# Optimization experiments

Measured on AMD Instinct MI355X. Metric: run time of the kernel, lower is better.

The kernel has to match this reference:

```python
import jax, jax.numpy as jnp
import numpy as np

ADAPTIVE_FACTOR = 10  # max(10, num_agents=8)


def _mlp(x, W1, b1, W2, b2, W3, b3):
    h = jax.nn.relu(x @ W1 + b1)
    h = jax.nn.relu(h @ W2 + b2)
    return h @ W3 + b3


def setup_inputs() -> dict:
    key = jax.random.key(0)
    ks = jax.random.split(key, 8)
    B, T, N, D, A = 32, 512, 8, 256, 64
    obs = jax.random.normal(ks[0], (B, T, N, D), dtype=jnp.float32)
    actions = jax.random.uniform(ks[1], (B, T, N, A), dtype=jnp.float32)
    din = D + A
    W1 = jax.random.normal(ks[2], (din, 128), dtype=jnp.float32) / np.sqrt(din)
    b1 = jnp.zeros((128,), dtype=jnp.float32)
    W2 = jax.random.normal(ks[3], (128, 64), dtype=jnp.float32) / np.sqrt(128.0)
    b2 = jnp.zeros((64,), dtype=jnp.float32)
    W3 = jax.random.normal(ks[4], (64, A), dtype=jnp.float32) / np.sqrt(64.0)
    b3 = jnp.zeros((A,), dtype=jnp.float32)
    return {"obs": obs, "actions": actions, "W1": W1, "b1": b1,
            "W2": W2, "b2": b2, "W3": W3, "b3": b3}


def reference(obs, actions, W1, b1, W2, b2, W3, b3):
    # obs: [B,T,N,D], actions: [B,T,N,A]. All agents processed in one batched MLP
    # pass instead of the per-agent Python loop in the original.
    p_with = _mlp(jnp.concatenate([obs, actions], axis=-1), W1, b1, W2, b2, W3, b3)
    p_wo = _mlp(jnp.concatenate([obs, jnp.zeros_like(actions)], axis=-1),
                W1, b1, W2, b2, W3, b3)

    cf_keys = jax.random.split(jax.random.key(42), ADAPTIVE_FACTOR)

    def body(acc, k):
        cf = jax.random.uniform(k, actions.shape, dtype=actions.dtype)
        return acc + _mlp(jnp.concatenate([obs, cf], axis=-1), W1, b1, W2, b2, W3, b3), None

    p_wo, _ = jax.lax.scan(body, p_wo, cf_keys)
    p_wo = p_wo / (ADAPTIVE_FACTOR + 1)

    # F.kl_div(log_softmax(p_with), softmax(p_wo), reduction='none')
    #   = q * (log q - log p)
    logp = jax.nn.log_softmax(p_with, axis=-1)
    logq = jax.nn.log_softmax(p_wo, axis=-1)
    q = jnp.exp(logq)
    influence = q * (logq - logp)          # [B,T,N,A]
    # torch: stack over agents on dim=-1 -> [B,T,A,N], then mean over dim=2 (A)
    return influence.mean(axis=-1)          # [B,T,N]
```

## Files before the change

kernel.cpp:

```cpp
#include <hip/hip_runtime.h>
#include <cstddef>

#define NCF 10

struct TFKeys { unsigned k[2 * NCF]; };

typedef __attribute__((ext_vector_type(8))) _Float16 f16x8;
typedef __attribute__((ext_vector_type(4))) float f32x4;

__host__ __device__ __forceinline__ void tf2x32(unsigned k0, unsigned k1,
                                                unsigned x0, unsigned x1,
                                                unsigned& o0, unsigned& o1) {
  const unsigned ks2 = k0 ^ k1 ^ 0x1BD11BDAu;
  x0 += k0; x1 += k1;
#define TF_R(r) x0 += x1; x1 = (x1 << (r)) | (x1 >> (32 - (r))); x1 ^= x0;
  TF_R(13) TF_R(15) TF_R(26) TF_R(6)
  x0 += k1;  x1 += ks2 + 1u;
  TF_R(17) TF_R(29) TF_R(16) TF_R(24)
  x0 += ks2; x1 += k0 + 2u;
  TF_R(13) TF_R(15) TF_R(26) TF_R(6)
  x0 += k0;  x1 += k1 + 3u;
  TF_R(17) TF_R(29) TF_R(16) TF_R(24)
  x0 += k1;  x1 += ks2 + 4u;
  TF_R(13) TF_R(15) TF_R(26) TF_R(6)
  x0 += ks2; x1 += k0 + 5u;
#undef TF_R
  o0 = x0; o1 = x1;
}

__device__ __forceinline__ float u01(unsigned bits) {
  return __uint_as_float((bits >> 9) | 0x3f800000u) - 1.0f;
}

__device__ __forceinline__ void split44(const float4 a, const float4 b,
                                        f16x8& hh, f16x8& ll) {
  const float v[8] = {a.x, a.y, a.z, a.w, b.x, b.y, b.z, b.w};
#pragma unroll
  for (int e = 0; e < 8; ++e) {
    const _Float16 h = (_Float16)v[e];
    hh[e] = h;
    ll[e] = (_Float16)(v[e] - (float)h);
  }
}

#define MFMA3(acc, ah, al, bh, bl)                                          \
  acc = __builtin_amdgcn_mfma_f32_16x16x32_f16(ah, bh, acc, 0, 0, 0);       \
  acc = __builtin_amdgcn_mfma_f32_16x16x32_f16(ah, bl, acc, 0, 0, 0);       \
  acc = __builtin_amdgcn_mfma_f32_16x16x32_f16(al, bh, acc, 0, 0, 0);

template <int K, int N>
__device__ __forceinline__ void stage_frags(const float* __restrict__ W,
                                            _Float16* fh, _Float16* fl, int t) {
  constexpr int NTN = N / 16;
  for (int i = t; i < K * N; i += 512) {
    const int e = i & 7, lane = (i >> 3) & 63, tile = i >> 9;
    const int kt = tile / NTN, nt = tile % NTN;
    const int k = kt * 32 + ((lane >> 4) << 3) + e;
    const int c = nt * 16 + (lane & 15);
    const float w = W[k * N + c];
    const _Float16 h = (_Float16)w;
    fh[i] = h;
    fl[i] = (_Float16)(w - (float)h);
  }
}

__global__ __launch_bounds__(512, 2) __attribute__((amdgpu_waves_per_eu(2, 2)))
void infl_fused(const float* __restrict__ obs, const float* __restrict__ actions,
                const float* __restrict__ W1, const float* __restrict__ b1,
                const float* __restrict__ W2, const float* __restrict__ b2,
                const float* __restrict__ W3, const float* __restrict__ b3,
                float* __restrict__ out, TFKeys keys) {
  __shared__ __align__(16) unsigned char smem[149504];
  _Float16* w1oh = (_Float16*)smem;
  _Float16* w1ol = (_Float16*)(smem + 65536);
  _Float16* w1h  = (_Float16*)smem;
  _Float16* w1l  = (_Float16*)(smem + 16384);
  _Float16* w2h  = (_Float16*)(smem + 32768);
  _Float16* w2l  = (_Float16*)(smem + 49152);
  _Float16* w3h  = (_Float16*)(smem + 65536);
  _Float16* w3l  = (_Float16*)(smem + 73728);
  float*    hbuf = (float*)(smem + 81920);

  const int t = threadIdx.x, wave = t >> 6, lane = t & 63;
  const int R0 = blockIdx.x * 128 + wave * 16;
  const int cA = lane & 15;
  const int kg = (lane >> 4) << 3;
  const int r0 = (lane >> 4) << 2;
  float* hb = hbuf + wave * 2112;

  stage_frags<256, 128>(W1, w1oh, w1ol, t);
  __syncthreads();

  f32x4 ho[8];
#pragma unroll
  for (int nt = 0; nt < 8; ++nt) {
    const float bv = b1[nt * 16 + cA];
    ho[nt] = (f32x4){bv, bv, bv, bv};
  }
  {
    const float* orow = obs + (size_t)(R0 + cA) * 256;
    float4 ov[16];
#pragma unroll
    for (int kt = 0; kt < 8; ++kt) {
      ov[2 * kt]     = *(const float4*)(orow + kt * 32 + kg);
      ov[2 * kt + 1] = *(const float4*)(orow + kt * 32 + kg + 4);
    }
#pragma unroll
    for (int kt = 0; kt < 8; ++kt) {
      f16x8 ah, al;
      split44(ov[2 * kt], ov[2 * kt + 1], ah, al);
#pragma unroll
      for (int nt = 0; nt < 8; ++nt) {
        const int tile = kt * 8 + nt;
        const f16x8 bh = *(const f16x8*)&w1oh[(tile * 64 + lane) * 8];
        const f16x8 bl = *(const f16x8*)&w1ol[(tile * 64 + lane) * 8];
        MFMA3(ho[nt], ah, al, bh, bl)
      }
    }
  }
  __syncthreads();

  stage_frags<64, 128>(W1 + 256 * 128, w1h, w1l, t);
  stage_frags<128, 64>(W2, w2h, w2l, t);
  stage_frags<64, 64>(W3, w3h, w3l, t);

  float b2r[4], b3r[4];
#pragma unroll
  for (int nt = 0; nt < 4; ++nt) {
    b2r[nt] = b2[nt * 16 + cA];
    b3r[nt] = b3[nt * 16 + cA];
  }
  __syncthreads();

#define MLP_BODY(HAS_ACT, acc3)                                              \
  {                                                                          \
    f32x4 a1[8];                                                             \
    _Pragma("unroll") for (int nt = 0; nt < 8; ++nt) a1[nt] = ho[nt];        \
    if (HAS_ACT) {                                                           \
      _Pragma("unroll") for (int kt = 0; kt < 2; ++kt)                       \
      _Pragma("unroll") for (int nt = 0; nt < 8; ++nt) {                     \
        const int tile = kt * 8 + nt;                                        \
        const f16x8 bh = *(const f16x8*)&w1h[(tile * 64 + lane) * 8];        \
        const f16x8 bl = *(const f16x8*)&w1l[(tile * 64 + lane) * 8];        \
        MFMA3(a1[nt], ah[kt], al[kt], bh, bl)                                \
      }                                                                      \
    }                                                                        \
    _Pragma("unroll") for (int nt = 0; nt < 8; ++nt)                         \
    _Pragma("unroll") for (int j = 0; j < 4; ++j)                            \
      hb[(r0 + j) * 132 + nt * 16 + cA] = fmaxf(a1[nt][j], 0.f);             \
    f32x4 a2[4];                                                             \
    _Pragma("unroll") for (int nt = 0; nt < 4; ++nt)                         \
      a2[nt] = (f32x4){b2r[nt], b2r[nt], b2r[nt], b2r[nt]};                  \
    _Pragma("unroll") for (int kt = 0; kt < 4; ++kt) {                       \
      const float4 va = *(const float4*)&hb[cA * 132 + kt * 32 + kg];        \
      const float4 vb = *(const float4*)&hb[cA * 132 + kt * 32 + kg + 4];    \
      f16x8 hh, hl;                                                          \
      split44(va, vb, hh, hl);                                               \
      _Pragma("unroll") for (int nt = 0; nt < 4; ++nt) {                     \
        const int tile = kt * 4 + nt;                                        \
        const f16x8 bh = *(const f16x8*)&w2h[(tile * 64 + lane) * 8];        \
        const f16x8 bl = *(const f16x8*)&w2l[(tile * 64 + lane) * 8];        \
        MFMA3(a2[nt], hh, hl, bh, bl)                                        \
      }                                                                      \
    }                                                                        \
    _Pragma("unroll") for (int nt = 0; nt < 4; ++nt)                         \
    _Pragma("unroll") for (int j = 0; j < 4; ++j)                            \
      hb[(r0 + j) * 68 + nt * 16 + cA] = fmaxf(a2[nt][j], 0.f);              \
    _Pragma("unroll") for (int kt = 0; kt < 2; ++kt) {                       \
      const float4 va = *(const float4*)&hb[cA * 68 + kt * 32 + kg];         \
      const float4 vb = *(const float4*)&hb[cA * 68 + kt * 32 + kg + 4];     \
      f16x8 hh, hl;                                                          \
      split44(va, vb, hh, hl);                                               \
      _Pragma("unroll") for (int nt = 0; nt < 4; ++nt) {                     \
        const int tile = kt * 4 + nt;                                        \
        const f16x8 bh = *(const f16x8*)&w3h[(tile * 64 + lane) * 8];        \
        const f16x8 bl = *(const f16x8*)&w3l[(tile * 64 + lane) * 8];        \
        MFMA3(acc3[nt], hh, hl, bh, bl)                                      \
      }                                                                      \
    }                                                                        \
  }

  f32x4 pacc[4];
#pragma unroll
  for (int nt = 0; nt < 4; ++nt) pacc[nt] = (f32x4){0.f, 0.f, 0.f, 0.f};

  for (int p = 0; p < 11; ++p) {
    f16x8 ah[2], al[2];
    if (p >= 1) {
      const unsigned k0 = keys.k[2 * (p - 1)];
      const unsigned k1 = keys.k[2 * (p - 1) + 1];
      const unsigned base = (unsigned)(R0 + cA) * 64u + (unsigned)kg;
#pragma unroll
      for (int kt = 0; kt < 2; ++kt) {
        float v[8];
#pragma unroll
        for (int e = 0; e < 8; ++e) {
          unsigned o0, o1;
          tf2x32(k0, k1, 0u, base + (unsigned)(kt * 32 + e), o0, o1);
          v[e] = u01(o0 ^ o1);
        }
        split44(*(const float4*)&v[0], *(const float4*)&v[4], ah[kt], al[kt]);
      }
    }
    MLP_BODY(p != 0, pacc)
  }

  f32x4 pw[4];
#pragma unroll
  for (int nt = 0; nt < 4; ++nt) pw[nt] = (f32x4){0.f, 0.f, 0.f, 0.f};
  {
    f16x8 ah[2], al[2];
    const float* arow = actions + (size_t)(R0 + cA) * 64 + kg;
#pragma unroll
    for (int kt = 0; kt < 2; ++kt) {
      const float4 va = *(const float4*)(arow + kt * 32);
      const float4 vb = *(const float4*)(arow + kt * 32 + 4);
      split44(va, vb, ah[kt], al[kt]);
    }
    MLP_BODY(true, pw)
  }

  const float inv11 = 1.0f / 11.0f;
#pragma unroll
  for (int j = 0; j < 4; ++j) {
    float pwv[4], pav[4];
#pragma unroll
    for (int nt = 0; nt < 4; ++nt) {
      pwv[nt] = pw[nt][j] + b3r[nt];
      pav[nt] = pacc[nt][j] * inv11 + b3r[nt];
    }
    float mw = fmaxf(fmaxf(pwv[0], pwv[1]), fmaxf(pwv[2], pwv[3]));
    float ma = fmaxf(fmaxf(pav[0], pav[1]), fmaxf(pav[2], pav[3]));
#pragma unroll
    for (int off = 1; off < 16; off <<= 1) {
      mw = fmaxf(mw, __shfl_xor(mw, off, 64));
      ma = fmaxf(ma, __shfl_xor(ma, off, 64));
    }
    float sw = 0.f, sa = 0.f;
#pragma unroll
    for (int nt = 0; nt < 4; ++nt) {
      sw += expf(pwv[nt] - mw);
      sa += expf(pav[nt] - ma);
    }
#pragma unroll
    for (int off = 1; off < 16; off <<= 1) {
      sw += __shfl_xor(sw, off, 64);
      sa += __shfl_xor(sa, off, 64);
    }
    const float lzw = logf(sw), lza = logf(sa);
    float contrib = 0.f;
#pragma unroll
    for (int nt = 0; nt < 4; ++nt) {
      const float lq = pav[nt] - ma - lza;
      const float lp = pwv[nt] - mw - lzw;
      contrib += expf(lq) * (lq - lp);
    }
#pragma unroll
    for (int off = 1; off < 16; off <<= 1)
      contrib += __shfl_xor(contrib, off, 64);
    if (cA == 0) out[R0 + r0 + j] = contrib * (1.0f / 64.0f);
  }
}

extern "C" void kernel_launch(void* const* d_in, const int* in_sizes, int n_in,
                              void* d_out, int out_size, void* d_ws, size_t ws_size,
                              hipStream_t stream) {
  (void)in_sizes; (void)n_in; (void)d_ws; (void)ws_size; (void)out_size;
  const float* obs     = (const float*)d_in[0];
  const float* actions = (const float*)d_in[1];
  const float* W1      = (const float*)d_in[2];
  const float* b1      = (const float*)d_in[3];
  const float* W2      = (const float*)d_in[4];
  const float* b2      = (const float*)d_in[5];
  const float* W3      = (const float*)d_in[6];
  const float* b3      = (const float*)d_in[7];

  TFKeys keys;
  for (unsigned j = 0; j < NCF; ++j) {
    unsigned o0, o1;
    tf2x32(0u, 42u, 0u, j, o0, o1);
    keys.k[2 * j]     = o0;
    keys.k[2 * j + 1] = o1;
  }

  hipLaunchKernelGGL(infl_fused, dim3(1024), dim3(512), 0, stream,
                     obs, actions, W1, b1, W2, b2, W3, b3, (float*)d_out, keys);
}
```

Before: 594.5 us.

## Double block size, chunk hidden activations through small swizzled LDS buffer

Blocks grow to 1024 threads covering 256 rows, so each block stages the weight fragments once for twice as many rows. The obs-part of W1 is now staged in two halves to cut LDS footprint. The layer-1 to layer-2 and layer-2 to layer-3 handoff now streams 32-column chunks through a small per-wave XOR-swizzled buffer instead of writing full padded hidden rows. This lowers shared memory per block and interleaves layers, which may add register pressure under the tighter 1024-thread launch bound.

```diff
diff --git a/kernel.cpp b/kernel.cpp
--- a/kernel.cpp
+++ b/kernel.cpp
@@ -48,11 +48,11 @@
   acc = __builtin_amdgcn_mfma_f32_16x16x32_f16(ah, bl, acc, 0, 0, 0);       \
   acc = __builtin_amdgcn_mfma_f32_16x16x32_f16(al, bh, acc, 0, 0, 0);
 
-template <int K, int N>
+template <int K, int N, int NT>
 __device__ __forceinline__ void stage_frags(const float* __restrict__ W,
                                             _Float16* fh, _Float16* fl, int t) {
   constexpr int NTN = N / 16;
-  for (int i = t; i < K * N; i += 512) {
+  for (int i = t; i < K * N; i += NT) {
     const int e = i & 7, lane = (i >> 3) & 63, tile = i >> 9;
     const int kt = tile / NTN, nt = tile % NTN;
     const int k = kt * 32 + ((lane >> 4) << 3) + e;
@@ -64,32 +64,32 @@
   }
 }
 
-__global__ __launch_bounds__(512, 2) __attribute__((amdgpu_waves_per_eu(2, 2)))
+__device__ __forceinline__ int swz(int row, int col) {
+  return (row << 5) + (col ^ ((row & 7) << 2));
+}
+
+__global__ __launch_bounds__(1024, 4)
 void infl_fused(const float* __restrict__ obs, const float* __restrict__ actions,
                 const float* __restrict__ W1, const float* __restrict__ b1,
                 const float* __restrict__ W2, const float* __restrict__ b2,
                 const float* __restrict__ W3, const float* __restrict__ b3,
                 float* __restrict__ out, TFKeys keys) {
-  __shared__ __align__(16) unsigned char smem[149504];
+  __shared__ __align__(16) unsigned char smem[114688];
   _Float16* w1oh = (_Float16*)smem;
-  _Float16* w1ol = (_Float16*)(smem + 65536);
+  _Float16* w1ol = (_Float16*)(smem + 32768);
   _Float16* w1h  = (_Float16*)smem;
   _Float16* w1l  = (_Float16*)(smem + 16384);
   _Float16* w2h  = (_Float16*)(smem + 32768);
   _Float16* w2l  = (_Float16*)(smem + 49152);
   _Float16* w3h  = (_Float16*)(smem + 65536);
   _Float16* w3l  = (_Float16*)(smem + 73728);
-  float*    hbuf = (float*)(smem + 81920);
 
   const int t = threadIdx.x, wave = t >> 6, lane = t & 63;
-  const int R0 = blockIdx.x * 128 + wave * 16;
+  const int R0 = blockIdx.x * 256 + wave * 16;
   const int cA = lane & 15;
   const int kg = (lane >> 4) << 3;
   const int r0 = (lane >> 4) << 2;
-  float* hb = hbuf + wave * 2112;
-
-  stage_frags<256, 128>(W1, w1oh, w1ol, t);
-  __syncthreads();
+  float* cb = (float*)(smem + 81920 + wave * 2048);
 
   f32x4 ho[8];
 #pragma unroll
@@ -99,30 +99,31 @@
   }
   {
     const float* orow = obs + (size_t)(R0 + cA) * 256;
-    float4 ov[16];
-#pragma unroll
-    for (int kt = 0; kt < 8; ++kt) {
-      ov[2 * kt]     = *(const float4*)(orow + kt * 32 + kg);
-      ov[2 * kt + 1] = *(const float4*)(orow + kt * 32 + kg + 4);
-    }
-#pragma unroll
-    for (int kt = 0; kt < 8; ++kt) {
-      f16x8 ah, al;
-      split44(ov[2 * kt], ov[2 * kt + 1], ah, al);
-#pragma unroll
-      for (int nt = 0; nt < 8; ++nt) {
-        const int tile = kt * 8 + nt;
-        const f16x8 bh = *(const f16x8*)&w1oh[(tile * 64 + lane) * 8];
-        const f16x8 bl = *(const f16x8*)&w1ol[(tile * 64 + lane) * 8];
-        MFMA3(ho[nt], ah, al, bh, bl)
+    for (int half = 0; half < 2; ++half) {
+      __syncthreads();
+      stage_frags<128, 128, 1024>(W1 + half * 128 * 128, w1oh, w1ol, t);
+      __syncthreads();
+#pragma unroll
+      for (int kt = 0; kt < 4; ++kt) {
+        const float4 va = *(const float4*)(orow + half * 128 + kt * 32 + kg);
+        const float4 vb = *(const float4*)(orow + half * 128 + kt * 32 + kg + 4);
+        f16x8 oh, ol;
+        split44(va, vb, oh, ol);
+#pragma unroll
+        for (int nt = 0; nt < 8; ++nt) {
+          const int tile = kt * 8 + nt;
+          const f16x8 bh = *(const f16x8*)&w1oh[(tile * 64 + lane) * 8];
+          const f16x8 bl = *(const f16x8*)&w1ol[(tile * 64 + lane) * 8];
+          MFMA3(ho[nt], oh, ol, bh, bl)
+        }
       }
     }
   }
   __syncthreads();
 
-  stage_frags<64, 128>(W1 + 256 * 128, w1h, w1l, t);
-  stage_frags<128, 64>(W2, w2h, w2l, t);
-  stage_frags<64, 64>(W3, w3h, w3l, t);
+  stage_frags<64, 128, 1024>(W1 + 256 * 128, w1h, w1l, t);
+  stage_frags<128, 64, 1024>(W2, w2h, w2l, t);
+  stage_frags<64, 64, 1024>(W3, w3h, w3l, t);
 
   float b2r[4], b3r[4];
 #pragma unroll
@@ -134,48 +135,52 @@
 
 #define MLP_BODY(HAS_ACT, acc3)                                              \
   {                                                                          \
-    f32x4 a1[8];                                                             \
-    _Pragma("unroll") for (int nt = 0; nt < 8; ++nt) a1[nt] = ho[nt];        \
-    if (HAS_ACT) {                                                           \
-      _Pragma("unroll") for (int kt = 0; kt < 2; ++kt)                       \
-      _Pragma("unroll") for (int nt = 0; nt < 8; ++nt) {                     \
-        const int tile = kt * 8 + nt;                                        \
-        const f16x8 bh = *(const f16x8*)&w1h[(tile * 64 + lane) * 8];        \
-        const f16x8 bl = *(const f16x8*)&w1l[(tile * 64 + lane) * 8];        \
-        MFMA3(a1[nt], ah[kt], al[kt], bh, bl)                                \
-      }                                                                      \
-    }                                                                        \
-    _Pragma("unroll") for (int nt = 0; nt < 8; ++nt)                         \
-    _Pragma("unroll") for (int j = 0; j < 4; ++j)                            \
-      hb[(r0 + j) * 132 + nt * 16 + cA] = fmaxf(a1[nt][j], 0.f);             \
     f32x4 a2[4];                                                             \
-    _Pragma("unroll") for (int nt = 0; nt < 4; ++nt)                         \
-      a2[nt] = (f32x4){b2r[nt], b2r[nt], b2r[nt], b2r[nt]};                  \
-    _Pragma("unroll") for (int kt = 0; kt < 4; ++kt) {                       \
-      const float4 va = *(const float4*)&hb[cA * 132 + kt * 32 + kg];        \
-      const float4 vb = *(const float4*)&hb[cA * 132 + kt * 32 + kg + 4];    \
+    _Pragma("unroll") for (int n2 = 0; n2 < 4; ++n2)                         \
+      a2[n2] = (f32x4){b2r[n2], b2r[n2], b2r[n2], b2r[n2]};                  \
+    _Pragma("unroll") for (int c = 0; c < 4; ++c) {                          \
+      f32x4 a10 = ho[2 * c], a11 = ho[2 * c + 1];                            \
+      if (HAS_ACT) {                                                         \
+        _Pragma("unroll") for (int kt = 0; kt < 2; ++kt) {                   \
+          const int t0 = ((kt * 8 + 2 * c) * 64 + lane) * 8;                 \
+          const int t1 = ((kt * 8 + 2 * c + 1) * 64 + lane) * 8;             \
+          const f16x8 bh0 = *(const f16x8*)&w1h[t0];                         \
+          const f16x8 bl0 = *(const f16x8*)&w1l[t0];                         \
+          MFMA3(a10, ah[kt], al[kt], bh0, bl0)                               \
+          const f16x8 bh1 = *(const f16x8*)&w1h[t1];                         \
+          const f16x8 bl1 = *(const f16x8*)&w1l[t1];                         \
+          MFMA3(a11, ah[kt], al[kt], bh1, bl1)                               \
+        }                                                                    \
+      }                                                                      \
+      _Pragma("unroll") for (int j = 0; j < 4; ++j) {                        \
+        cb[swz(r0 + j, cA)]      = fmaxf(a10[j], 0.f);                       \
+        cb[swz(r0 + j, 16 + cA)] = fmaxf(a11[j], 0.f);                       \
+      }                                                                      \
+      const float4 va = *(const float4*)&cb[swz(cA, kg)];                    \
+      const float4 vb = *(const float4*)&cb[swz(cA, kg + 4)];                \
       f16x8 hh, hl;                                                          \
       split44(va, vb, hh, hl);                                               \
-      _Pragma("unroll") for (int nt = 0; nt < 4; ++nt) {                     \
-        const int tile = kt * 4 + nt;                                        \
-        const f16x8 bh = *(const f16x8*)&w2h[(tile * 64 + lane) * 8];        \
-        const f16x8 bl = *(const f16x8*)&w2l[(tile * 64 + lane) * 8];        \
-        MFMA3(a2[nt], hh, hl, bh, bl)                                        \
+      _Pragma("unroll") for (int n2 = 0; n2 < 4; ++n2) {                     \
+        const int tt = ((c * 4 + n2) * 64 + lane) * 8;                       \
+        const f16x8 bh = *(const f16x8*)&w2h[tt];                            \
+        const f16x8 bl = *(const f16x8*)&w2l[tt];                            \
+        MFMA3(a2[n2], hh, hl, bh, bl)                                        \
       }                                                                      \
     }                                                                        \
-    _Pragma("unroll") for (int nt = 0; nt < 4; ++nt)                         \
-    _Pragma("unroll") for (int j = 0; j < 4; ++j)                            \
-      hb[(r0 + j) * 68 + nt * 16 + cA] = fmaxf(a2[nt][j], 0.f);              \
-    _Pragma("unroll") for (int kt = 0; kt < 2; ++kt) {                       \
-      const float4 va = *(const float4*)&hb[cA * 68 + kt * 32 + kg];         \
-      const float4 vb = *(const float4*)&hb[cA * 68 + kt * 32 + kg + 4];     \
+    _Pragma("unroll") for (int d = 0; d < 2; ++d) {                          \
+      _Pragma("unroll") for (int j = 0; j < 4; ++j) {                        \
+        cb[swz(r0 + j, cA)]      = fmaxf(a2[2 * d][j], 0.f);                 \
+        cb[swz(r0 + j, 16 + cA)] = fmaxf(a2[2 * d + 1][j], 0.f);             \
+      }                                                                      \
+      const float4 va = *(const float4*)&cb[swz(cA, kg)];                    \
+      const float4 vb = *(const float4*)&cb[swz(cA, kg + 4)];                \
       f16x8 hh, hl;                                                          \
       split44(va, vb, hh, hl);                                               \
-      _Pragma("unroll") for (int nt = 0; nt < 4; ++nt) {                     \
-        const int tile = kt * 4 + nt;                                        \
-        const f16x8 bh = *(const f16x8*)&w3h[(tile * 64 + lane) * 8];        \
-        const f16x8 bl = *(const f16x8*)&w3l[(tile * 64 + lane) * 8];        \
-        MFMA3(acc3[nt], hh, hl, bh, bl)                                      \
+      _Pragma("unroll") for (int n3 = 0; n3 < 4; ++n3) {                     \
+        const int tt = ((d * 4 + n3) * 64 + lane) * 8;                       \
+        const f16x8 bh = *(const f16x8*)&w3h[tt];                            \
+        const f16x8 bl = *(const f16x8*)&w3l[tt];                            \
+        MFMA3(acc3[n3], hh, hl, bh, bl)                                      \
       }                                                                      \
     }                                                                        \
   }
@@ -283,6 +288,6 @@
     keys.k[2 * j + 1] = o1;
   }
 
-  hipLaunchKernelGGL(infl_fused, dim3(1024), dim3(512), 0, stream,
+  hipLaunchKernelGGL(infl_fused, dim3(512), dim3(1024), 0, stream,
                      obs, actions, W1, b1, W2, b2, W3, b3, (float*)d_out, keys);
 }
```

After: 827.1 us. 39.1% more time.
